# Kernel tuning notes

Measured on AMD Instinct MI355X. Metric: run time of the kernel, lower is better.

The kernel has to match this reference:

```python
import jax, jax.numpy as jnp
import numpy as np

IN_CH = 1024
OUT_CH = 1024
BATCH = 4096


def setup_inputs() -> dict:
    key = jax.random.key(0)
    ks = jax.random.split(key, 8)
    s = 1.0 / np.sqrt(IN_CH)
    return {
        "hidden_rep": jax.random.normal(ks[0], (1, BATCH, IN_CH), jnp.float32),
        "W_ih": jax.random.uniform(ks[1], (3 * IN_CH, IN_CH), jnp.float32, -s, s),
        "W_hh": jax.random.uniform(ks[2], (3 * IN_CH, IN_CH), jnp.float32, -s, s),
        "b_ih": jax.random.uniform(ks[3], (3 * IN_CH,), jnp.float32, -s, s),
        "b_hh": jax.random.uniform(ks[4], (3 * IN_CH,), jnp.float32, -s, s),
        "W_out": jax.random.uniform(ks[5], (OUT_CH, IN_CH), jnp.float32, -s, s),
        "b_out": jax.random.uniform(ks[6], (OUT_CH,), jnp.float32, -s, s),
        "max_try": 16,
    }


def _gru_cell(x, h, W_ih, W_hh, b_ih, b_hh):
    # x, h: (B, H). PyTorch GRU gate ordering: reset, update, new.
    gi = x @ W_ih.T + b_ih  # (B, 3H)
    gh = h @ W_hh.T + b_hh  # (B, 3H)
    i_r, i_z, i_n = jnp.split(gi, 3, axis=-1)
    h_r, h_z, h_n = jnp.split(gh, 3, axis=-1)
    r = jax.nn.sigmoid(i_r + h_r)
    z = jax.nn.sigmoid(i_z + h_z)
    n = jnp.tanh(i_n + r * h_n)
    return (1.0 - z) * n + z * h


def reference(hidden_rep, W_ih, W_hh, b_ih, b_hh, W_out, b_out, max_try):
    h0 = hidden_rep[0]           # (B, H) initial hidden state
    x0 = jnp.zeros_like(h0)      # zeros_like(hidden_rep): first input is zeros

    def step(carry, _):
        x, h = carry
        h_new = _gru_cell(x, h, W_ih, W_hh, b_ih, b_hh)
        # seq output of single-layer GRU == new hidden; it is fed back as next input
        out = jax.nn.relu(h_new) @ W_out.T + b_out
        return (h_new, h_new), out

    _, outs = jax.lax.scan(step, (x0, h0), None, length=max_try)
    return outs  # (max_try, B, OUT_CH) == torch.cat(outputs, dim=0)
```

## Files before the change

### kernel.cpp

```cpp
#include <hip/hip_runtime.h>
#include <hip/hip_bf16.h>


#define H_DIM 1024
#define BATCH_N 4096
#define NSTEPS 16
#define K4 (4 * H_DIM)

typedef __bf16 bf16_t;
typedef __bf16 bf16x8 __attribute__((ext_vector_type(8)));
typedef float f32x4 __attribute__((ext_vector_type(4)));

__device__ __forceinline__ float sigm(float x) { return 1.0f / (1.0f + __expf(-x)); }


__global__ __launch_bounds__(256) void prep_weights(
    const float* __restrict__ Wih, const float* __restrict__ Whh,
    const float* __restrict__ bih, const float* __restrict__ bhh,
    const float* __restrict__ Wout,
    bf16_t* __restrict__ Wc0, bf16_t* __restrict__ Wc,
    bf16_t* __restrict__ Wob, float* __restrict__ biasc)
{
    const int stride = gridDim.x * blockDim.x;
    const int idx = blockIdx.x * blockDim.x + threadIdx.x;

    const int total = K4 * H_DIM;
    for (int i = idx; i < total; i += stride) {
        const int c2 = i >> 10;
        const int col = i & (H_DIM - 1);
        const int gate = (c2 >> 4) & 3;
        const int hc = ((c2 >> 6) << 4) | (c2 & 15);
        float vc, v0;
        if (gate == 0) {
            float a = Wih[(size_t)hc * H_DIM + col];
            float b = Whh[(size_t)hc * H_DIM + col];
            vc = a + b; v0 = b;
        } else if (gate == 1) {
            float a = Wih[(size_t)(H_DIM + hc) * H_DIM + col];
            float b = Whh[(size_t)(H_DIM + hc) * H_DIM + col];
            vc = a + b; v0 = b;
        } else if (gate == 2) {
            vc = Wih[(size_t)(2 * H_DIM + hc) * H_DIM + col];
            v0 = 0.0f;
        } else {
            float b = Whh[(size_t)(2 * H_DIM + hc) * H_DIM + col];
            vc = b; v0 = b;
        }
        Wc[i]  = (bf16_t)vc;
        Wc0[i] = (bf16_t)v0;
    }
    for (int i = idx; i < H_DIM * H_DIM; i += stride)
        Wob[i] = (bf16_t)Wout[i];
    for (int i = idx; i < K4; i += stride) {
        const int gate = i >> 10;
        const int hc = i & (H_DIM - 1);
        float v;
        if (gate == 0)      v = bih[hc] + bhh[hc];
        else if (gate == 1) v = bih[H_DIM + hc] + bhh[H_DIM + hc];
        else if (gate == 2) v = bih[2 * H_DIM + hc];
        else                v = bhh[2 * H_DIM + hc];
        biasc[i] = v;
    }
}

__global__ __launch_bounds__(256) void prep_h(
    const float* __restrict__ h0, bf16_t* __restrict__ hb)
{
    const int stride = gridDim.x * blockDim.x;
    for (int i = blockIdx.x * blockDim.x + threadIdx.x; i < BATCH_N * H_DIM; i += stride)
        hb[i] = (bf16_t)h0[i];
}


__device__ __forceinline__ void stage_half(
    const bf16_t* __restrict__ g, int grow0, int K, int k0,
    bf16_t* ldsbase, int l)
{
    const int colsrc = (((l & 3) ^ ((l >> 3) & 3)) << 3);
    const bf16_t* ga = g + (size_t)(grow0 + (l >> 2)) * K + k0 + colsrc;
    __builtin_amdgcn_global_load_lds(
        (const __attribute__((address_space(1))) void*)ga,
        (__attribute__((address_space(3))) void*)ldsbase, 16, 0, 0);
}

template <bool FUSED>
__global__ __launch_bounds__(512, 2) void gemm256(
    const bf16_t* __restrict__ A, const bf16_t* __restrict__ Bm,
    int M, int N, int K,
    float* __restrict__ C, const float* __restrict__ bias,
    const float* __restrict__ biasc,
    bf16_t* __restrict__ hbout, bf16_t* __restrict__ hr)
{
    __shared__ bf16_t lds[65536];

    const int tid = threadIdx.x;
    const int l = tid & 63;
    const int w = tid >> 6;
    const int wr = w >> 2;
    const int wc = w & 3;

    int bx, by;
    if constexpr (FUSED) {
        const int d = blockIdx.x;
        const int r = d & 7, s = d >> 3;
        bx = (r & 3) * 4 + (s & 3);
        by = (r >> 2) * 8 + (s >> 2);
    } else {
        const int nbx = N >> 8;
        const int cpx = gridDim.x >> 3;
        const int d = blockIdx.x;
        const int bid = (d & 7) * cpx + (d >> 3);
        bx = bid % nbx;
        by = bid / nbx;
    }
    const int brow = by * 256;
    const int bcol = bx * 256;

    f32x4 acc[8][4];
    const f32x4 zero = {0.f, 0.f, 0.f, 0.f};
#pragma unroll
    for (int m = 0; m < 8; ++m)
#pragma unroll
        for (int n = 0; n < 4; ++n) acc[m][n] = zero;

    const int Z = K >> 5;

#define STAGE_A(zz) do { \
    bf16_t* lb_ = lds + ((zz) & 3) * 16384 + w * 512; \
    stage_half(A, brow + w * 16, K, (zz) * 32, lb_, l); \
    stage_half(A, brow + 128 + w * 16, K, (zz) * 32, lb_ + 4096, l); \
} while (0)
#define STAGE_B(zz) do { \
    bf16_t* lb_ = lds + ((zz) & 3) * 16384 + 8192 + w * 512; \
    stage_half(Bm, bcol + w * 16, K, (zz) * 32, lb_, l); \
    stage_half(Bm, bcol + 128 + w * 16, K, (zz) * 32, lb_ + 4096, l); \
} while (0)

    STAGE_A(0); STAGE_B(0);
    STAGE_A(1); STAGE_B(1);
    STAGE_A(2); STAGE_B(2);

    const int colrd = (((l >> 4) ^ ((l >> 1) & 3)) << 3);
    const int ar0 = (wr * 128 + (l & 15)) * 32 + colrd;
    const int br0 = 8192 + (wc * 64 + (l & 15)) * 32 + colrd;

    bf16x8 afrag[4], bfrag[4];
    for (int z = 0; z < Z; ++z) {
        if (z + 2 < Z)      asm volatile("s_waitcnt vmcnt(8)" ::: "memory");
        else if (z + 1 < Z) asm volatile("s_waitcnt vmcnt(4)" ::: "memory");
        else                asm volatile("s_waitcnt vmcnt(0)" ::: "memory");
        __builtin_amdgcn_s_barrier();

        const int sb = (z & 3) * 16384;

#pragma unroll
        for (int n = 0; n < 4; ++n)
            bfrag[n] = *(const bf16x8*)&lds[sb + br0 + n * 512];
#pragma unroll
        for (int m = 0; m < 4; ++m)
            afrag[m] = *(const bf16x8*)&lds[sb + ar0 + m * 512];
        if (z + 3 < Z) STAGE_A(z + 3);

        __builtin_amdgcn_s_setprio(1);
#pragma unroll
        for (int m = 0; m < 4; ++m)
#pragma unroll
            for (int n = 0; n < 4; ++n)
                acc[m][n] = __builtin_amdgcn_mfma_f32_16x16x32_bf16(afrag[m], bfrag[n], acc[m][n], 0, 0, 0);
        __builtin_amdgcn_s_setprio(0);

        bf16x8 afrag2[4];
#pragma unroll
        for (int m = 0; m < 4; ++m)
            afrag2[m] = *(const bf16x8*)&lds[sb + ar0 + (m + 4) * 512];
        if (z + 3 < Z) STAGE_B(z + 3);

        __builtin_amdgcn_s_setprio(1);
#pragma unroll
        for (int m = 0; m < 4; ++m)
#pragma unroll
            for (int n = 0; n < 4; ++n)
                acc[m + 4][n] = __builtin_amdgcn_mfma_f32_16x16x32_bf16(afrag2[m], bfrag[n], acc[m + 4][n], 0, 0, 0);
        __builtin_amdgcn_s_setprio(0);
    }
#undef STAGE_A
#undef STAGE_B

    if constexpr (FUSED) {
        const int hc = (bx * 4 + wc) * 16 + (l & 15);
        const float br_ = biasc[hc];
        const float bz_ = biasc[H_DIM + hc];
        const float bi_ = biasc[2 * H_DIM + hc];
        const float bh_ = biasc[3 * H_DIM + hc];
        const int r0 = brow + wr * 128 + ((l >> 4) << 2);
#pragma unroll
        for (int m = 0; m < 8; ++m) {
#pragma unroll
            for (int j = 0; j < 4; ++j) {
                const int row = r0 + m * 16 + j;
                const size_t o = (size_t)row * H_DIM + hc;
                const float hold = (float)A[o];
                const float r = sigm(acc[m][0][j] + br_);
                const float z = sigm(acc[m][1][j] + bz_);
                float a = acc[m][2][j] + bi_ + r * (acc[m][3][j] + bh_);
                a = fminf(fmaxf(a, -30.f), 30.f);
                const float e = __expf(-2.f * a);
                const float nn = (1.f - e) / (1.f + e);
                const float hn = (1.f - z) * nn + z * hold;
                hbout[o] = (bf16_t)hn;
                hr[o] = (bf16_t)fmaxf(hn, 0.f);
            }
        }
    } else {
        const int r0 = brow + wr * 128 + ((l >> 4) << 2);
        const int c0 = bcol + wc * 64 + (l & 15);
#pragma unroll
        for (int m = 0; m < 8; ++m) {
#pragma unroll
            for (int n = 0; n < 4; ++n) {
                const int col = c0 + n * 16;
                const float badd = bias ? bias[col] : 0.0f;
#pragma unroll
                for (int j = 0; j < 4; ++j) {
                    const int row = r0 + m * 16 + j;
                    C[(size_t)row * N + col] = acc[m][n][j] + badd;
                }
            }
        }
    }
}


extern "C" void kernel_launch(void* const* d_in, const int* in_sizes, int n_in,
                              void* d_out, int out_size, void* d_ws, size_t ws_size,
                              hipStream_t stream)
{
    const float* hidden = (const float*)d_in[0];
    const float* Wih = (const float*)d_in[1];
    const float* Whh = (const float*)d_in[2];
    const float* bih = (const float*)d_in[3];
    const float* bhh = (const float*)d_in[4];
    const float* Wout = (const float*)d_in[5];
    const float* bout = (const float*)d_in[6];
    float* out = (float*)d_out;
    (void)in_sizes; (void)n_in; (void)out_size;

    char* ws = (char*)d_ws;
    size_t off = 0;
    bf16_t* Wc0 = (bf16_t*)(ws + off); off += (size_t)K4 * H_DIM * 2;
    bf16_t* Wc  = (bf16_t*)(ws + off); off += (size_t)K4 * H_DIM * 2;
    bf16_t* Wob = (bf16_t*)(ws + off); off += (size_t)H_DIM * H_DIM * 2;
    float*  biasc = (float*)(ws + off); off += (size_t)K4 * 4;
    bf16_t* hbA = (bf16_t*)(ws + off); off += (size_t)BATCH_N * H_DIM * 2;
    bf16_t* hbB = (bf16_t*)(ws + off); off += (size_t)BATCH_N * H_DIM * 2;

    const size_t hr_step = (size_t)BATCH_N * H_DIM;
    const size_t need_batched = off + NSTEPS * hr_step * 2;
    const bool batched = (ws_size >= need_batched);
    bf16_t* hr_all = (bf16_t*)(ws + off);

    prep_weights<<<1024, 256, 0, stream>>>(Wih, Whh, bih, bhh, Wout, Wc0, Wc, Wob, biasc);
    prep_h<<<2048, 256, 0, stream>>>(hidden, hbA);

    for (int t = 0; t < NSTEPS; ++t) {
        bf16_t* hin  = (t & 1) ? hbB : hbA;
        bf16_t* hout = (t & 1) ? hbA : hbB;
        bf16_t* hr_t = batched ? (hr_all + (size_t)t * hr_step) : hr_all;
        gemm256<true><<<(BATCH_N / 256) * (K4 / 256), 512, 0, stream>>>(
            hin, (t == 0) ? Wc0 : Wc, BATCH_N, K4, H_DIM,
            nullptr, nullptr, biasc, hout, hr_t);
        if (!batched) {
            gemm256<false><<<(BATCH_N / 256) * (H_DIM / 256), 512, 0, stream>>>(
                hr_t, Wob, BATCH_N, H_DIM, H_DIM,
                out + (size_t)t * hr_step, bout, nullptr, nullptr, nullptr);
        }
    }
    if (batched) {
        gemm256<false><<<((NSTEPS * BATCH_N) / 256) * (H_DIM / 256), 512, 0, stream>>>(
            hr_all, Wob, NSTEPS * BATCH_N, H_DIM, H_DIM,
            out, bout, nullptr, nullptr, nullptr);
    }
}
```

Before: 768.9 us.

## Switch GEMM core from 16x16x32 to 32x32x16 bf16 MFMA tiles

```diff
diff --git a/kernel.cpp b/kernel.cpp
--- a/kernel.cpp
+++ b/kernel.cpp
@@ -9,7 +9,7 @@
 
 typedef __bf16 bf16_t;
 typedef __bf16 bf16x8 __attribute__((ext_vector_type(8)));
-typedef float f32x4 __attribute__((ext_vector_type(4)));
+typedef float f32x16 __attribute__((ext_vector_type(16)));
 
 __device__ __forceinline__ float sigm(float x) { return 1.0f / (1.0f + __expf(-x)); }
 
@@ -28,8 +28,8 @@
     for (int i = idx; i < total; i += stride) {
         const int c2 = i >> 10;
         const int col = i & (H_DIM - 1);
-        const int gate = (c2 >> 4) & 3;
-        const int hc = ((c2 >> 6) << 4) | (c2 & 15);
+        const int gate = (c2 >> 5) & 3;
+        const int hc = ((c2 >> 7) << 5) | (c2 & 31);
         float vc, v0;
         if (gate == 0) {
             float a = Wih[(size_t)hc * H_DIM + col];
@@ -96,8 +96,10 @@
     const int tid = threadIdx.x;
     const int l = tid & 63;
     const int w = tid >> 6;
-    const int wr = w >> 2;
-    const int wc = w & 3;
+    const int wrM = w >> 1;
+    const int wcN = w & 1;
+    const int lanecol = l & 31;
+    const int hi = l >> 5;
 
     int bx, by;
     if constexpr (FUSED) {
@@ -116,12 +118,13 @@
     const int brow = by * 256;
     const int bcol = bx * 256;
 
-    f32x4 acc[8][4];
-    const f32x4 zero = {0.f, 0.f, 0.f, 0.f};
-#pragma unroll
-    for (int m = 0; m < 8; ++m)
-#pragma unroll
-        for (int n = 0; n < 4; ++n) acc[m][n] = zero;
+    f32x16 acc[2][4];
+#pragma unroll
+    for (int m = 0; m < 2; ++m)
+#pragma unroll
+        for (int n = 0; n < 4; ++n)
+#pragma unroll
+            for (int r = 0; r < 16; ++r) acc[m][n][r] = 0.f;
 
     const int Z = K >> 5;
 
@@ -140,11 +143,24 @@
     STAGE_A(1); STAGE_B(1);
     STAGE_A(2); STAGE_B(2);
 
-    const int colrd = (((l >> 4) ^ ((l >> 1) & 3)) << 3);
-    const int ar0 = (wr * 128 + (l & 15)) * 32 + colrd;
-    const int br0 = 8192 + (wc * 64 + (l & 15)) * 32 + colrd;
-
-    bf16x8 afrag[4], bfrag[4];
+    int aoff[2][2], boff[4][2];
+#pragma unroll
+    for (int m = 0; m < 2; ++m) {
+        const int arow = wrM * 64 + m * 32 + lanecol;
+        const int g = (arow >> 1) & 3;
+#pragma unroll
+        for (int ks = 0; ks < 2; ++ks)
+            aoff[m][ks] = arow * 32 + (((ks * 2 + hi) ^ g) << 3);
+    }
+#pragma unroll
+    for (int n = 0; n < 4; ++n) {
+        const int brw = wcN * 128 + n * 32 + lanecol;
+        const int g = (brw >> 1) & 3;
+#pragma unroll
+        for (int ks = 0; ks < 2; ++ks)
+            boff[n][ks] = 8192 + brw * 32 + (((ks * 2 + hi) ^ g) << 3);
+    }
+
     for (int z = 0; z < Z; ++z) {
         if (z + 2 < Z)      asm volatile("s_waitcnt vmcnt(8)" ::: "memory");
         else if (z + 1 < Z) asm volatile("s_waitcnt vmcnt(4)" ::: "memory");
@@ -153,77 +169,80 @@
 
         const int sb = (z & 3) * 16384;
 
+        bf16x8 afrag[2][2], bfrag[4][2];
 #pragma unroll
         for (int n = 0; n < 4; ++n)
-            bfrag[n] = *(const bf16x8*)&lds[sb + br0 + n * 512];
-#pragma unroll
-        for (int m = 0; m < 4; ++m)
-            afrag[m] = *(const bf16x8*)&lds[sb + ar0 + m * 512];
+#pragma unroll
+            for (int ks = 0; ks < 2; ++ks)
+                bfrag[n][ks] = *(const bf16x8*)&lds[sb + boff[n][ks]];
+#pragma unroll
+        for (int m = 0; m < 2; ++m)
+#pragma unroll
+            for (int ks = 0; ks < 2; ++ks)
+                afrag[m][ks] = *(const bf16x8*)&lds[sb + aoff[m][ks]];
         if (z + 3 < Z) STAGE_A(z + 3);
 
         __builtin_amdgcn_s_setprio(1);
 #pragma unroll
-        for (int m = 0; m < 4; ++m)
+        for (int m = 0; m < 2; ++m)
 #pragma unroll
             for (int n = 0; n < 4; ++n)
-                acc[m][n] = __builtin_amdgcn_mfma_f32_16x16x32_bf16(afrag[m], bfrag[n], acc[m][n], 0, 0, 0);
+                acc[m][n] = __builtin_amdgcn_mfma_f32_32x32x16_bf16(
+                    afrag[m][0], bfrag[n][0], acc[m][n], 0, 0, 0);
         __builtin_amdgcn_s_setprio(0);
 
-        bf16x8 afrag2[4];
-#pragma unroll
-        for (int m = 0; m < 4; ++m)
-            afrag2[m] = *(const bf16x8*)&lds[sb + ar0 + (m + 4) * 512];
         if (z + 3 < Z) STAGE_B(z + 3);
 
         __builtin_amdgcn_s_setprio(1);
 #pragma unroll
-        for (int m = 0; m < 4; ++m)
+        for (int m = 0; m < 2; ++m)
 #pragma unroll
             for (int n = 0; n < 4; ++n)
-                acc[m + 4][n] = __builtin_amdgcn_mfma_f32_16x16x32_bf16(afrag2[m], bfrag[n], acc[m + 4][n], 0, 0, 0);
+                acc[m][n] = __builtin_amdgcn_mfma_f32_32x32x16_bf16(
+                    afrag[m][1], bfrag[n][1], acc[m][n], 0, 0, 0);
         __builtin_amdgcn_s_setprio(0);
     }
 #undef STAGE_A
 #undef STAGE_B
 
     if constexpr (FUSED) {
-        const int hc = (bx * 4 + wc) * 16 + (l & 15);
+        const int hc = ((bcol >> 7) + wcN) * 32 + lanecol;
         const float br_ = biasc[hc];
         const float bz_ = biasc[H_DIM + hc];
         const float bi_ = biasc[2 * H_DIM + hc];
         const float bh_ = biasc[3 * H_DIM + hc];
-        const int r0 = brow + wr * 128 + ((l >> 4) << 2);
-#pragma unroll
-        for (int m = 0; m < 8; ++m) {
-#pragma unroll
-            for (int j = 0; j < 4; ++j) {
-                const int row = r0 + m * 16 + j;
+        const int rbase = brow + wrM * 64 + hi * 4;
+#pragma unroll
+        for (int m = 0; m < 2; ++m) {
+#pragma unroll
+            for (int r = 0; r < 16; ++r) {
+                const int row = rbase + m * 32 + (r & 3) + 8 * (r >> 2);
                 const size_t o = (size_t)row * H_DIM + hc;
                 const float hold = (float)A[o];
-                const float r = sigm(acc[m][0][j] + br_);
-                const float z = sigm(acc[m][1][j] + bz_);
-                float a = acc[m][2][j] + bi_ + r * (acc[m][3][j] + bh_);
+                const float rr = sigm(acc[m][0][r] + br_);
+                const float zz = sigm(acc[m][1][r] + bz_);
+                float a = acc[m][2][r] + bi_ + rr * (acc[m][3][r] + bh_);
                 a = fminf(fmaxf(a, -30.f), 30.f);
                 const float e = __expf(-2.f * a);
                 const float nn = (1.f - e) / (1.f + e);
-                const float hn = (1.f - z) * nn + z * hold;
+                const float hn = (1.f - zz) * nn + zz * hold;
                 hbout[o] = (bf16_t)hn;
                 hr[o] = (bf16_t)fmaxf(hn, 0.f);
             }
         }
     } else {
-        const int r0 = brow + wr * 128 + ((l >> 4) << 2);
-        const int c0 = bcol + wc * 64 + (l & 15);
-#pragma unroll
-        for (int m = 0; m < 8; ++m) {
-#pragma unroll
-            for (int n = 0; n < 4; ++n) {
-                const int col = c0 + n * 16;
-                const float badd = bias ? bias[col] : 0.0f;
-#pragma unroll
-                for (int j = 0; j < 4; ++j) {
-                    const int row = r0 + m * 16 + j;
-                    C[(size_t)row * N + col] = acc[m][n][j] + badd;
+        const int r0 = brow + wrM * 64 + hi * 4;
+        const int c0 = bcol + wcN * 128 + lanecol;
+#pragma unroll
+        for (int n = 0; n < 4; ++n) {
+            const int col = c0 + n * 32;
+            const float badd = bias ? bias[col] : 0.0f;
+#pragma unroll
+            for (int m = 0; m < 2; ++m) {
+#pragma unroll
+                for (int r = 0; r < 16; ++r) {
+                    const int row = r0 + m * 32 + (r & 3) + 8 * (r >> 2);
+                    C[(size_t)row * N + col] = acc[m][n][r] + badd;
                 }
             }
         }
```

After: 840.6 us. 9.3% more time.

## Switch GEMM to 128x256 tiles with 4 waves and triple-buffered LDS

Applied to the files above, without the earlier changes.

```diff
diff --git a/kernel.cpp b/kernel.cpp
--- a/kernel.cpp
+++ b/kernel.cpp
@@ -84,82 +84,77 @@
 }
 
 template <bool FUSED>
-__global__ __launch_bounds__(512, 2) void gemm256(
+__global__ __launch_bounds__(256, 2) void gemm128(
     const bf16_t* __restrict__ A, const bf16_t* __restrict__ Bm,
     int M, int N, int K,
     float* __restrict__ C, const float* __restrict__ bias,
     const float* __restrict__ biasc,
     bf16_t* __restrict__ hbout, bf16_t* __restrict__ hr)
 {
-    __shared__ bf16_t lds[65536];
+    __shared__ bf16_t lds[36864];
 
     const int tid = threadIdx.x;
     const int l = tid & 63;
     const int w = tid >> 6;
-    const int wr = w >> 2;
-    const int wc = w & 3;
-
-    int bx, by;
-    if constexpr (FUSED) {
-        const int d = blockIdx.x;
-        const int r = d & 7, s = d >> 3;
-        bx = (r & 3) * 4 + (s & 3);
-        by = (r >> 2) * 8 + (s >> 2);
-    } else {
-        const int nbx = N >> 8;
-        const int cpx = gridDim.x >> 3;
-        const int d = blockIdx.x;
-        const int bid = (d & 7) * cpx + (d >> 3);
-        bx = bid % nbx;
-        by = bid / nbx;
-    }
-    const int brow = by * 256;
+    const int wrM = w >> 1;
+    const int wcN = w & 1;
+
+    const int nbx = N >> 8;
+    const int cpx = gridDim.x >> 3;
+    const int d = blockIdx.x;
+    const int bid = (d & 7) * cpx + (d >> 3);
+    const int bx = bid % nbx;
+    const int by = bid / nbx;
+    const int brow = by * 128;
     const int bcol = bx * 256;
 
-    f32x4 acc[8][4];
+    f32x4 acc[4][8];
     const f32x4 zero = {0.f, 0.f, 0.f, 0.f};
 #pragma unroll
-    for (int m = 0; m < 8; ++m)
-#pragma unroll
-        for (int n = 0; n < 4; ++n) acc[m][n] = zero;
+    for (int m = 0; m < 4; ++m)
+#pragma unroll
+        for (int n = 0; n < 8; ++n) acc[m][n] = zero;
 
     const int Z = K >> 5;
 
-#define STAGE_A(zz) do { \
-    bf16_t* lb_ = lds + ((zz) & 3) * 16384 + w * 512; \
-    stage_half(A, brow + w * 16, K, (zz) * 32, lb_, l); \
-    stage_half(A, brow + 128 + w * 16, K, (zz) * 32, lb_ + 4096, l); \
+#define STAGE_A(zz, base) do { \
+    stage_half(A, brow + w * 16, K, (zz) * 32, (base) + (w * 16) * 32, l); \
+    stage_half(A, brow + 64 + w * 16, K, (zz) * 32, (base) + (64 + w * 16) * 32, l); \
 } while (0)
-#define STAGE_B(zz) do { \
-    bf16_t* lb_ = lds + ((zz) & 3) * 16384 + 8192 + w * 512; \
-    stage_half(Bm, bcol + w * 16, K, (zz) * 32, lb_, l); \
-    stage_half(Bm, bcol + 128 + w * 16, K, (zz) * 32, lb_ + 4096, l); \
+#define STAGE_B(zz, base) do { \
+    stage_half(Bm, bcol + w * 16, K, (zz) * 32, (base) + 4096 + (w * 16) * 32, l); \
+    stage_half(Bm, bcol + 64 + w * 16, K, (zz) * 32, (base) + 4096 + (64 + w * 16) * 32, l); \
+    stage_half(Bm, bcol + 128 + w * 16, K, (zz) * 32, (base) + 4096 + (128 + w * 16) * 32, l); \
+    stage_half(Bm, bcol + 192 + w * 16, K, (zz) * 32, (base) + 4096 + (192 + w * 16) * 32, l); \
 } while (0)
 
-    STAGE_A(0); STAGE_B(0);
-    STAGE_A(1); STAGE_B(1);
-    STAGE_A(2); STAGE_B(2);
+    STAGE_A(0, lds);
+    STAGE_B(0, lds);
+    STAGE_A(1, lds + 12288);
+    STAGE_B(1, lds + 12288);
 
     const int colrd = (((l >> 4) ^ ((l >> 1) & 3)) << 3);
-    const int ar0 = (wr * 128 + (l & 15)) * 32 + colrd;
-    const int br0 = 8192 + (wc * 64 + (l & 15)) * 32 + colrd;
-
-    bf16x8 afrag[4], bfrag[4];
+    const int ar0 = (wrM * 64 + (l & 15)) * 32 + colrd;
+    const int br0 = 4096 + (wcN * 128 + (l & 15)) * 32 + colrd;
+
+    int slot = 0;
     for (int z = 0; z < Z; ++z) {
-        if (z + 2 < Z)      asm volatile("s_waitcnt vmcnt(8)" ::: "memory");
-        else if (z + 1 < Z) asm volatile("s_waitcnt vmcnt(4)" ::: "memory");
-        else                asm volatile("s_waitcnt vmcnt(0)" ::: "memory");
+        if (z + 1 < Z) asm volatile("s_waitcnt vmcnt(6)" ::: "memory");
+        else           asm volatile("s_waitcnt vmcnt(0)" ::: "memory");
         __builtin_amdgcn_s_barrier();
 
-        const int sb = (z & 3) * 16384;
-
-#pragma unroll
-        for (int n = 0; n < 4; ++n)
+        const int sb = slot * 12288;
+        int s2 = slot + 2; if (s2 >= 3) s2 -= 3;
+        bf16_t* stbase = lds + s2 * 12288;
+
+        bf16x8 afrag[4], bfrag[8];
+#pragma unroll
+        for (int n = 0; n < 8; ++n)
             bfrag[n] = *(const bf16x8*)&lds[sb + br0 + n * 512];
 #pragma unroll
         for (int m = 0; m < 4; ++m)
             afrag[m] = *(const bf16x8*)&lds[sb + ar0 + m * 512];
-        if (z + 3 < Z) STAGE_A(z + 3);
+        if (z + 2 < Z) STAGE_A(z + 2, stbase);
 
         __builtin_amdgcn_s_setprio(1);
 #pragma unroll
@@ -169,57 +164,59 @@
                 acc[m][n] = __builtin_amdgcn_mfma_f32_16x16x32_bf16(afrag[m], bfrag[n], acc[m][n], 0, 0, 0);
         __builtin_amdgcn_s_setprio(0);
 
-        bf16x8 afrag2[4];
+        if (z + 2 < Z) STAGE_B(z + 2, stbase);
+
+        __builtin_amdgcn_s_setprio(1);
 #pragma unroll
         for (int m = 0; m < 4; ++m)
-            afrag2[m] = *(const bf16x8*)&lds[sb + ar0 + (m + 4) * 512];
-        if (z + 3 < Z) STAGE_B(z + 3);
-
-        __builtin_amdgcn_s_setprio(1);
-#pragma unroll
-        for (int m = 0; m < 4; ++m)
-#pragma unroll
-            for (int n = 0; n < 4; ++n)
-                acc[m + 4][n] = __builtin_amdgcn_mfma_f32_16x16x32_bf16(afrag2[m], bfrag[n], acc[m + 4][n], 0, 0, 0);
+#pragma unroll
+            for (int n = 4; n < 8; ++n)
+                acc[m][n] = __builtin_amdgcn_mfma_f32_16x16x32_bf16(afrag[m], bfrag[n], acc[m][n], 0, 0, 0);
         __builtin_amdgcn_s_setprio(0);
+
+        slot = (slot + 1 == 3) ? 0 : slot + 1;
     }
 #undef STAGE_A
 #undef STAGE_B
 
     if constexpr (FUSED) {
-        const int hc = (bx * 4 + wc) * 16 + (l & 15);
-        const float br_ = biasc[hc];
-        const float bz_ = biasc[H_DIM + hc];
-        const float bi_ = biasc[2 * H_DIM + hc];
-        const float bh_ = biasc[3 * H_DIM + hc];
-        const int r0 = brow + wr * 128 + ((l >> 4) << 2);
-#pragma unroll
-        for (int m = 0; m < 8; ++m) {
-#pragma unroll
-            for (int j = 0; j < 4; ++j) {
-                const int row = r0 + m * 16 + j;
-                const size_t o = (size_t)row * H_DIM + hc;
-                const float hold = (float)A[o];
-                const float r = sigm(acc[m][0][j] + br_);
-                const float z = sigm(acc[m][1][j] + bz_);
-                float a = acc[m][2][j] + bi_ + r * (acc[m][3][j] + bh_);
-                a = fminf(fmaxf(a, -30.f), 30.f);
-                const float e = __expf(-2.f * a);
-                const float nn = (1.f - e) / (1.f + e);
-                const float hn = (1.f - z) * nn + z * hold;
-                hbout[o] = (bf16_t)hn;
-                hr[o] = (bf16_t)fmaxf(hn, 0.f);
+        const int hcb = (bcol >> 6) + wcN * 2;
+        const int r0 = brow + wrM * 64 + ((l >> 4) << 2);
+#pragma unroll
+        for (int hcg = 0; hcg < 2; ++hcg) {
+            const int hc = (hcb + hcg) * 16 + (l & 15);
+            const float br_ = biasc[hc];
+            const float bz_ = biasc[H_DIM + hc];
+            const float bi_ = biasc[2 * H_DIM + hc];
+            const float bh_ = biasc[3 * H_DIM + hc];
+#pragma unroll
+            for (int m = 0; m < 4; ++m) {
+#pragma unroll
+                for (int j = 0; j < 4; ++j) {
+                    const int row = r0 + m * 16 + j;
+                    const size_t o = (size_t)row * H_DIM + hc;
+                    const float hold = (float)A[o];
+                    const float rr = sigm(acc[m][hcg * 4 + 0][j] + br_);
+                    const float zz = sigm(acc[m][hcg * 4 + 1][j] + bz_);
+                    float a = acc[m][hcg * 4 + 2][j] + bi_ + rr * (acc[m][hcg * 4 + 3][j] + bh_);
+                    a = fminf(fmaxf(a, -30.f), 30.f);
+                    const float e = __expf(-2.f * a);
+                    const float nn = (1.f - e) / (1.f + e);
+                    const float hn = (1.f - zz) * nn + zz * hold;
+                    hbout[o] = (bf16_t)hn;
+                    hr[o] = (bf16_t)fmaxf(hn, 0.f);
+                }
             }
         }
     } else {
-        const int r0 = brow + wr * 128 + ((l >> 4) << 2);
-        const int c0 = bcol + wc * 64 + (l & 15);
-#pragma unroll
-        for (int m = 0; m < 8; ++m) {
-#pragma unroll
-            for (int n = 0; n < 4; ++n) {
-                const int col = c0 + n * 16;
-                const float badd = bias ? bias[col] : 0.0f;
+        const int r0 = brow + wrM * 64 + ((l >> 4) << 2);
+        const int c0 = bcol + wcN * 128 + (l & 15);
+#pragma unroll
+        for (int n = 0; n < 8; ++n) {
+            const int col = c0 + n * 16;
+            const float badd = bias ? bias[col] : 0.0f;
+#pragma unroll
+            for (int m = 0; m < 4; ++m) {
 #pragma unroll
                 for (int j = 0; j < 4; ++j) {
                     const int row = r0 + m * 16 + j;
@@ -266,17 +263,17 @@
         bf16_t* hin  = (t & 1) ? hbB : hbA;
         bf16_t* hout = (t & 1) ? hbA : hbB;
         bf16_t* hr_t = batched ? (hr_all + (size_t)t * hr_step) : hr_all;
-        gemm256<true><<<(BATCH_N / 256) * (K4 / 256), 512, 0, stream>>>(
+        gemm128<true><<<(BATCH_N / 128) * (K4 / 256), 256, 0, stream>>>(
             hin, (t == 0) ? Wc0 : Wc, BATCH_N, K4, H_DIM,
             nullptr, nullptr, biasc, hout, hr_t);
         if (!batched) {
-            gemm256<false><<<(BATCH_N / 256) * (H_DIM / 256), 512, 0, stream>>>(
+            gemm128<false><<<(BATCH_N / 128) * (H_DIM / 256), 256, 0, stream>>>(
                 hr_t, Wob, BATCH_N, H_DIM, H_DIM,
                 out + (size_t)t * hr_step, bout, nullptr, nullptr, nullptr);
         }
     }
     if (batched) {
-        gemm256<false><<<((NSTEPS * BATCH_N) / 256) * (H_DIM / 256), 512, 0, stream>>>(
+        gemm128<false><<<((NSTEPS * BATCH_N) / 128) * (H_DIM / 256), 256, 0, stream>>>(
             hr_all, Wob, NSTEPS * BATCH_N, H_DIM, H_DIM,
             out, bout, nullptr, nullptr, nullptr);
     }
```

Measured after the change: 845.3 us. 9.9% more time.
